# Kernel tuning notes

Hardware: AMD Instinct MI355X
Metric: run time of the kernel (lower is better)

The kernel has to match this reference:

```python
import jax, jax.numpy as jnp
import numpy as np

B, T, I, H = 16384, 512, 1, 8  # batch, seq_len, input_size, hidden_size


def setup_inputs() -> dict:
    key = jax.random.key(0)
    ks = jax.random.split(key, 11)
    s = 0.1  # weight init scale
    return {
        "x": jax.random.normal(ks[0], (B, T, I), jnp.float32),
        "h0": jax.random.normal(ks[1], (2, B, H), jnp.float32),
        "c0": jax.random.normal(ks[2], (2, B, H), jnp.float32),
        "w_ih_f": jax.random.normal(ks[3], (4 * H, I), jnp.float32) * s,
        "w_hh_f": jax.random.normal(ks[4], (4 * H, H), jnp.float32) * s,
        "b_f": jax.random.normal(ks[5], (4 * H,), jnp.float32) * s,
        "w_ih_b": jax.random.normal(ks[6], (4 * H, I), jnp.float32) * s,
        "w_hh_b": jax.random.normal(ks[7], (4 * H, H), jnp.float32) * s,
        "b_b": jax.random.normal(ks[8], (4 * H,), jnp.float32) * s,
        "w_lin": jax.random.normal(ks[9], (1, 2 * H), jnp.float32) * s,
        "b_lin": jax.random.normal(ks[10], (1,), jnp.float32) * s,
    }


def _lstm_dir(x_tbi, h0, c0, w_ih, w_hh, b):
    """Single-direction LSTM over time-major input (T,B,I). PyTorch gate order i,f,g,o."""
    def step(carry, xt):
        h, c = carry
        z = xt @ w_ih.T + h @ w_hh.T + b  # (B, 4H)
        i, f, g, o = jnp.split(z, 4, axis=-1)
        c = jax.nn.sigmoid(f) * c + jax.nn.sigmoid(i) * jnp.tanh(g)
        h = jax.nn.sigmoid(o) * jnp.tanh(c)
        return (h, c), h

    _, hs = jax.lax.scan(step, (h0, c0), x_tbi)
    return hs  # (T, B, H)


def reference(x, h0, c0, w_ih_f, w_hh_f, b_f, w_ih_b, w_hh_b, b_b, w_lin, b_lin):
    xt = jnp.swapaxes(x, 0, 1)  # (T, B, I)
    hs_f = _lstm_dir(xt, h0[0], c0[0], w_ih_f, w_hh_f, b_f)
    hs_b = _lstm_dir(xt[::-1], h0[1], c0[1], w_ih_b, w_hh_b, b_b)
    # output[:, -1, :] = [fwd hidden at t=T-1, bwd hidden at t=T-1].
    # The bwd direction's state at time index T-1 is its FIRST scan output.
    last = jnp.concatenate([hs_f[-1], hs_b[0]], axis=-1)  # (B, 2H)
    return last @ w_lin.T + b_lin  # (B, 1)
```

## Files before the change

kernel.cpp:

```cpp
#include <hip/hip_runtime.h>


#define LOG2E 1.4426950408889634f

typedef __fp16 h2 __attribute__((ext_vector_type(2)));

#define DPPF(v, ctrl) __int_as_float(__builtin_amdgcn_update_dpp(0, __float_as_int(v), (ctrl), 0xF, 0xF, true))
#define DPPQH(v, k) __builtin_bit_cast(h2, __builtin_amdgcn_update_dpp(0, __builtin_bit_cast(int, (v)), ((k) * 0x55), 0xF, 0xF, true))

struct Ctx {
    h2 wi2[4], wf2[4], wg2[4], wo2[4];
    float xi, xf, xg, xo;
    float bi, bf, bg, bo;
};

__device__ __forceinline__ void load_ctx(Ctx& C, int j, int qp,
    const float* __restrict__ w_ih, const float* __restrict__ w_hh,
    const float* __restrict__ b)
{
    const float si = -LOG2E;
    const float sg = 2.0f * LOG2E;

    const float* ri = w_hh + (size_t)j * 8;
    const float* rf = w_hh + (size_t)(8 + j) * 8;
    const float* rg = w_hh + (size_t)(16 + j) * 8;
    const float* ro = w_hh + (size_t)(24 + j) * 8;
#pragma unroll
    for (int p = 0; p < 4; ++p) {
        int s0 = 4 * qp + p;
        int s1 = 7 - 4 * qp - p;
        C.wi2[p] = h2{(__fp16)(ri[s0] * si), (__fp16)(ri[s1] * si)};
        C.wf2[p] = h2{(__fp16)(rf[s0] * si), (__fp16)(rf[s1] * si)};
        C.wg2[p] = h2{(__fp16)(rg[s0] * sg), (__fp16)(rg[s1] * sg)};
        C.wo2[p] = h2{(__fp16)(ro[s0] * si), (__fp16)(ro[s1] * si)};
    }
    C.xi = w_ih[j] * si;      C.bi = b[j] * si;
    C.xf = w_ih[8 + j] * si;  C.bf = b[8 + j] * si;
    C.xg = w_ih[16 + j] * sg; C.bg = b[16 + j] * sg;
    C.xo = w_ih[24 + j] * si; C.bo = b[24 + j] * si;
}

__device__ __forceinline__ void lstm_step(float xt, float& h, float& cs, const Ctx& C)
{
    float hm = DPPF(h, 0x141);
    h2 ph = __builtin_amdgcn_cvt_pkrtz(h, hm);
    h2 p0 = DPPQH(ph, 0);
    h2 p1 = DPPQH(ph, 1);
    h2 p2 = DPPQH(ph, 2);
    h2 p3 = DPPQH(ph, 3);

    float zi = fmaf(xt, C.xi, C.bi);
    float zf = fmaf(xt, C.xf, C.bf);
    float zg = fmaf(xt, C.xg, C.bg);
    float zo = fmaf(xt, C.xo, C.bo);
    zi = __builtin_amdgcn_fdot2(p0, C.wi2[0], zi, false);
    zf = __builtin_amdgcn_fdot2(p0, C.wf2[0], zf, false);
    zg = __builtin_amdgcn_fdot2(p0, C.wg2[0], zg, false);
    zo = __builtin_amdgcn_fdot2(p0, C.wo2[0], zo, false);
    zi = __builtin_amdgcn_fdot2(p1, C.wi2[1], zi, false);
    zf = __builtin_amdgcn_fdot2(p1, C.wf2[1], zf, false);
    zg = __builtin_amdgcn_fdot2(p1, C.wg2[1], zg, false);
    zo = __builtin_amdgcn_fdot2(p1, C.wo2[1], zo, false);
    zi = __builtin_amdgcn_fdot2(p2, C.wi2[2], zi, false);
    zf = __builtin_amdgcn_fdot2(p2, C.wf2[2], zf, false);
    zg = __builtin_amdgcn_fdot2(p2, C.wg2[2], zg, false);
    zo = __builtin_amdgcn_fdot2(p2, C.wo2[2], zo, false);
    zi = __builtin_amdgcn_fdot2(p3, C.wi2[3], zi, false);
    zf = __builtin_amdgcn_fdot2(p3, C.wf2[3], zf, false);
    zg = __builtin_amdgcn_fdot2(p3, C.wg2[3], zg, false);
    zo = __builtin_amdgcn_fdot2(p3, C.wo2[3], zo, false);

    float eg = __builtin_amdgcn_exp2f(zg);
    float ei = __builtin_amdgcn_exp2f(zi);
    float ef = __builtin_amdgcn_exp2f(zf);
    float eo = __builtin_amdgcn_exp2f(zo);
    float di = 1.0f + ei, df = 1.0f + ef;
    float dg = 1.0f + eg, dz = 1.0f + eo;

    float d12 = di * df;
    float d34 = dg * dz;
    float R = __builtin_amdgcn_rcpf(d12 * d34);
    float t34 = R * d34;
    float t12 = R * d12;
    float sigi = t34 * df;
    float sigf = t34 * di;
    float qg   = t12 * dz;
    float sigo = t12 * dg;

    float tgs = fmaf(-4.0f * LOG2E, qg, 2.0f * LOG2E);
    cs = fmaf(sigf, cs, sigi * tgs);
    float ec = __builtin_amdgcn_exp2f(cs);
    float qc = __builtin_amdgcn_rcpf(1.0f + ec);
    h = sigo * fmaf(-2.0f, qc, 1.0f);
}

__global__ __launch_bounds__(256, 2) void bilstm_kernel(
    const float* __restrict__ x, const float* __restrict__ h0, const float* __restrict__ c0,
    const float* __restrict__ w_ih_f, const float* __restrict__ w_hh_f, const float* __restrict__ b_f,
    const float* __restrict__ w_ih_b, const float* __restrict__ w_hh_b, const float* __restrict__ b_b,
    const float* __restrict__ w_lin, const float* __restrict__ b_lin,
    float* __restrict__ out, int B, int T)
{
    int tid = blockIdx.x * 256 + threadIdx.x;
    int b = tid >> 3;
    int j = tid & 7;
    int qp = (threadIdx.x >> 2) & 1;
    if (b >= B) return;

    Ctx Cf;
    load_ctx(Cf, j, qp, w_ih_f, w_hh_f, b_f);

    float h  = h0[(size_t)b * 8 + j];
    float cs = c0[(size_t)b * 8 + j] * (2.0f * LOG2E);

    const float4* xr = (const float4*)(x + (size_t)b * T);
    int nT4 = T >> 2;
    float4 xv = xr[0];
    for (int t4 = 0; t4 < nT4 - 1; ++t4) {
        float4 nxt = xr[t4 + 1];
        lstm_step(xv.x, h, cs, Cf);
        lstm_step(xv.y, h, cs, Cf);
        lstm_step(xv.z, h, cs, Cf);
        lstm_step(xv.w, h, cs, Cf);
        xv = nxt;
    }
    lstm_step(xv.x, h, cs, Cf);
    lstm_step(xv.y, h, cs, Cf);
    lstm_step(xv.z, h, cs, Cf);
    float xlast = xv.w;
    lstm_step(xlast, h, cs, Cf);

    Ctx Cb;
    load_ctx(Cb, j, qp, w_ih_b, w_hh_b, b_b);
    float hb  = h0[(size_t)B * 8 + (size_t)b * 8 + j];
    float cbs = c0[(size_t)B * 8 + (size_t)b * 8 + j] * (2.0f * LOG2E);
    lstm_step(xlast, hb, cbs, Cb);

    float part = fmaf(h, w_lin[j], hb * w_lin[8 + j]);
    part += __shfl_xor(part, 1, 8);
    part += __shfl_xor(part, 2, 8);
    part += __shfl_xor(part, 4, 8);
    if (j == 0) out[b] = part + b_lin[0];
}

extern "C" void kernel_launch(void* const* d_in, const int* in_sizes, int n_in,
                              void* d_out, int out_size, void* d_ws, size_t ws_size,
                              hipStream_t stream)
{
    const float* x      = (const float*)d_in[0];
    const float* h0     = (const float*)d_in[1];
    const float* c0     = (const float*)d_in[2];
    const float* w_ih_f = (const float*)d_in[3];
    const float* w_hh_f = (const float*)d_in[4];
    const float* b_f    = (const float*)d_in[5];
    const float* w_ih_b = (const float*)d_in[6];
    const float* w_hh_b = (const float*)d_in[7];
    const float* b_b    = (const float*)d_in[8];
    const float* w_lin  = (const float*)d_in[9];
    const float* b_lin  = (const float*)d_in[10];
    float* out = (float*)d_out;

    int B = in_sizes[1] / 16;
    int T = in_sizes[0] / B;

    int threads = B * 8;
    dim3 block(256);
    dim3 grid((threads + 255) / 256);
    hipLaunchKernelGGL(bilstm_kernel, grid, block, 0, stream,
                       x, h0, c0, w_ih_f, w_hh_f, b_f, w_ih_b, w_hh_b, b_b,
                       w_lin, b_lin, out, B, T);
}
```

Measured before the change: 117.0 us.

## Process two batch elements per thread group to interleave independent recurrences

Each group of 8 threads now runs two independent batch sequences and interleaves their LSTM steps, giving the scheduler two dependency chains to overlap latency. The grid is halved and launch bounds relaxed to allow more registers. In exchange, there are fewer waves and occupancy drops, so hiding latency now depends on ILP rather than wave count. It also assumes B is even.

```diff
diff --git a/kernel.cpp b/kernel.cpp
--- a/kernel.cpp
+++ b/kernel.cpp
@@ -40,7 +40,7 @@
     C.xo = w_ih[24 + j] * si; C.bo = b[24 + j] * si;
 }
 
-__device__ __forceinline__ void lstm_step(float xt, float& h, float& cs, const Ctx& C)
+__device__ __forceinline__ void lstm_step1(float xt, float& h, float& cs, const Ctx& C)
 {
     float hm = DPPF(h, 0x141);
     h2 ph = __builtin_amdgcn_cvt_pkrtz(h, hm);
@@ -94,7 +94,7 @@
     h = sigo * fmaf(-2.0f, qc, 1.0f);
 }
 
-__global__ __launch_bounds__(256, 2) void bilstm_kernel(
+__global__ __launch_bounds__(256, 1) void bilstm_kernel(
     const float* __restrict__ x, const float* __restrict__ h0, const float* __restrict__ c0,
     const float* __restrict__ w_ih_f, const float* __restrict__ w_hh_f, const float* __restrict__ b_f,
     const float* __restrict__ w_ih_b, const float* __restrict__ w_hh_b, const float* __restrict__ b_b,
@@ -102,45 +102,62 @@
     float* __restrict__ out, int B, int T)
 {
     int tid = blockIdx.x * 256 + threadIdx.x;
-    int b = tid >> 3;
+    int p = tid >> 3;
     int j = tid & 7;
     int qp = (threadIdx.x >> 2) & 1;
-    if (b >= B) return;
+    if (p >= (B >> 1)) return;
+    int e0 = 2 * p, e1 = 2 * p + 1;
 
     Ctx Cf;
     load_ctx(Cf, j, qp, w_ih_f, w_hh_f, b_f);
 
-    float h  = h0[(size_t)b * 8 + j];
-    float cs = c0[(size_t)b * 8 + j] * (2.0f * LOG2E);
+    float hA  = h0[(size_t)e0 * 8 + j];
+    float hB  = h0[(size_t)e1 * 8 + j];
+    float csA = c0[(size_t)e0 * 8 + j] * (2.0f * LOG2E);
+    float csB = c0[(size_t)e1 * 8 + j] * (2.0f * LOG2E);
 
-    const float4* xr = (const float4*)(x + (size_t)b * T);
+    const float4* xrA = (const float4*)(x + (size_t)e0 * T);
+    const float4* xrB = (const float4*)(x + (size_t)e1 * T);
     int nT4 = T >> 2;
-    float4 xv = xr[0];
+    float4 xvA = xrA[0];
+    float4 xvB = xrB[0];
     for (int t4 = 0; t4 < nT4 - 1; ++t4) {
-        float4 nxt = xr[t4 + 1];
-        lstm_step(xv.x, h, cs, Cf);
-        lstm_step(xv.y, h, cs, Cf);
-        lstm_step(xv.z, h, cs, Cf);
-        lstm_step(xv.w, h, cs, Cf);
-        xv = nxt;
+        float4 nA = xrA[t4 + 1];
+        float4 nB = xrB[t4 + 1];
+        lstm_step1(xvA.x, hA, csA, Cf); lstm_step1(xvB.x, hB, csB, Cf);
+        lstm_step1(xvA.y, hA, csA, Cf); lstm_step1(xvB.y, hB, csB, Cf);
+        lstm_step1(xvA.z, hA, csA, Cf); lstm_step1(xvB.z, hB, csB, Cf);
+        lstm_step1(xvA.w, hA, csA, Cf); lstm_step1(xvB.w, hB, csB, Cf);
+        xvA = nA; xvB = nB;
     }
-    lstm_step(xv.x, h, cs, Cf);
-    lstm_step(xv.y, h, cs, Cf);
-    lstm_step(xv.z, h, cs, Cf);
-    float xlast = xv.w;
-    lstm_step(xlast, h, cs, Cf);
+    lstm_step1(xvA.x, hA, csA, Cf); lstm_step1(xvB.x, hB, csB, Cf);
+    lstm_step1(xvA.y, hA, csA, Cf); lstm_step1(xvB.y, hB, csB, Cf);
+    lstm_step1(xvA.z, hA, csA, Cf); lstm_step1(xvB.z, hB, csB, Cf);
+    float xlastA = xvA.w, xlastB = xvB.w;
+    lstm_step1(xlastA, hA, csA, Cf); lstm_step1(xlastB, hB, csB, Cf);
 
     Ctx Cb;
     load_ctx(Cb, j, qp, w_ih_b, w_hh_b, b_b);
-    float hb  = h0[(size_t)B * 8 + (size_t)b * 8 + j];
-    float cbs = c0[(size_t)B * 8 + (size_t)b * 8 + j] * (2.0f * LOG2E);
-    lstm_step(xlast, hb, cbs, Cb);
+    float hbA  = h0[(size_t)B * 8 + (size_t)e0 * 8 + j];
+    float hbB  = h0[(size_t)B * 8 + (size_t)e1 * 8 + j];
+    float cbA  = c0[(size_t)B * 8 + (size_t)e0 * 8 + j] * (2.0f * LOG2E);
+    float cbB  = c0[(size_t)B * 8 + (size_t)e1 * 8 + j] * (2.0f * LOG2E);
+    lstm_step1(xlastA, hbA, cbA, Cb);
+    lstm_step1(xlastB, hbB, cbB, Cb);
 
-    float part = fmaf(h, w_lin[j], hb * w_lin[8 + j]);
-    part += __shfl_xor(part, 1, 8);
-    part += __shfl_xor(part, 2, 8);
-    part += __shfl_xor(part, 4, 8);
-    if (j == 0) out[b] = part + b_lin[0];
+    float pA = fmaf(hA, w_lin[j], hbA * w_lin[8 + j]);
+    float pB = fmaf(hB, w_lin[j], hbB * w_lin[8 + j]);
+    pA += __shfl_xor(pA, 1, 8);
+    pB += __shfl_xor(pB, 1, 8);
+    pA += __shfl_xor(pA, 2, 8);
+    pB += __shfl_xor(pB, 2, 8);
+    pA += __shfl_xor(pA, 4, 8);
+    pB += __shfl_xor(pB, 4, 8);
+    if (j == 0) {
+        float bl = b_lin[0];
+        out[e0] = pA + bl;
+        out[e1] = pB + bl;
+    }
 }
 
 extern "C" void kernel_launch(void* const* d_in, const int* in_sizes, int n_in,
@@ -163,7 +180,7 @@
     int B = in_sizes[1] / 16;
     int T = in_sizes[0] / B;
 
-    int threads = B * 8;
+    int threads = (B / 2) * 8;
     dim3 block(256);
     dim3 grid((threads + 255) / 256);
     hipLaunchKernelGGL(bilstm_kernel, grid, block, 0, stream,
```

New measurement: 105.2 us (median of 2 runs). 10.1% less time.
